# Kernel tuning notes

Hardware: AMD Instinct MI355X
Metric: run time of the kernel (lower is better)

Reference implementation:

```python
import jax, jax.numpy as jnp
import numpy as np

N, QLEN, KLEN = 4, 2048, 2048
QDIM = KVDIM = 512
EMBED, HEADS = 1024, 16
HEAD_DIM = EMBED // HEADS


def setup_inputs() -> dict:
    key = jax.random.key(0)
    ks = jax.random.split(key, 7)
    return {
        "queries": jax.random.normal(ks[0], (N, QLEN, QDIM), dtype=jnp.float32),
        "keys": jax.random.normal(ks[1], (1, KLEN, KVDIM), dtype=jnp.float32),
        "values": jax.random.normal(ks[2], (1, KLEN, KVDIM), dtype=jnp.float32),
        "mask": jax.random.randint(ks[3], (N, 1, 1, KLEN), 0, 2, dtype=jnp.int32),
        "Wq": jax.random.normal(ks[4], (QDIM, EMBED), dtype=jnp.float32) * (QDIM ** -0.5),
        "Wk": jax.random.normal(ks[5], (KVDIM, EMBED), dtype=jnp.float32) * (KVDIM ** -0.5),
        "Wv": jax.random.normal(ks[6], (KVDIM, EMBED), dtype=jnp.float32) * (KVDIM ** -0.5),
    }


def reference(queries, keys, values, mask, Wq, Wk, Wv):
    # Projections (Linear, no bias)
    q = (queries @ Wq).reshape(N, QLEN, HEADS, HEAD_DIM)      # [N, Q, H, D]
    k = (keys @ Wk).reshape(KLEN, HEADS, HEAD_DIM)            # [K, H, D] (batch-1, shared)
    v = (values @ Wv).reshape(KLEN, HEADS, HEAD_DIM)          # [K, H, D]

    # energy: [N, H, Q, K]
    energy = jnp.einsum('nqhd,khd->nhqk', q, k)
    energy = jnp.where(mask == 0, jnp.float32(-1e20), energy)
    attn = jax.nn.softmax(energy / jnp.float32(HEAD_DIM ** 0.5), axis=3)

    out = jnp.einsum('nhqk,khd->nqhd', attn, v)               # [N, Q, H, D]
    return out.reshape(N, QLEN, EMBED)
```

## Files before the change

kernel.cpp:

```cpp
#include <hip/hip_runtime.h>

#define NB 4
#define QLEN 2048
#define KLEN 2048
#define QDIM 512
#define EMBED 1024
#define HEADS 16
#define HD 64

typedef __bf16 bf16x8 __attribute__((ext_vector_type(8)));
typedef float f32x2 __attribute__((ext_vector_type(2)));
typedef float f32x4 __attribute__((ext_vector_type(4)));
typedef float f32x16 __attribute__((ext_vector_type(16)));

#define CLOG 0.18033688011112042f

__device__ __forceinline__ float fexp2(float x) {
#if __has_builtin(__builtin_amdgcn_exp2f)
    return __builtin_amdgcn_exp2f(x);
#else
    float r;
    asm("v_exp_f32 %0, %1\n\ts_nop 1" : "=v"(r) : "v"(x));
    return r;
#endif
}

#if __has_builtin(__builtin_amdgcn_sched_barrier)
#define SCHED_FENCE() __builtin_amdgcn_sched_barrier(0)
#else
#define SCHED_FENCE()
#endif

__device__ __forceinline__ void dma16(const void* g, void* l) {
    __builtin_amdgcn_global_load_lds(
        (const __attribute__((address_space(1))) void*)g,
        (__attribute__((address_space(3))) void*)l, 16, 0, 0);
}

__global__ __launch_bounds__(256) void prep(const float* __restrict__ q,
                                            const float* __restrict__ k,
                                            const float* __restrict__ v,
                                            const float* __restrict__ Wq,
                                            const float* __restrict__ Wk,
                                            const float* __restrict__ Wv,
                                            const int* __restrict__ mask,
                                            __bf16* __restrict__ qd,
                                            __bf16* __restrict__ kd,
                                            __bf16* __restrict__ vd,
                                            __bf16* __restrict__ WtQ,
                                            __bf16* __restrict__ WtK,
                                            __bf16* __restrict__ WtV,
                                            int* __restrict__ pidx,
                                            int* __restrict__ cntg,
                                            __bf16* __restrict__ kbf,
                                            __bf16* __restrict__ vtbf) {
    __shared__ float tile[32][33];
    __shared__ int part[256];
    int b = blockIdx.x, tid = threadIdx.x;
    if (b >= 4612) {
        int t2 = b - 4612, n = t2 >> 4, h = t2 & 15;
        const int* mp = mask + n * KLEN + tid * 8;
        int4 ma = *(const int4*)&mp[0];
        int4 mb = *(const int4*)&mp[4];
        int c = (ma.x != 0) + (ma.y != 0) + (ma.z != 0) + (ma.w != 0)
              + (mb.x != 0) + (mb.y != 0) + (mb.z != 0) + (mb.w != 0);
        part[tid] = c;
        __syncthreads();
        for (int off = 128; off > 0; off >>= 1) {
            if (tid < off) part[tid] += part[tid + off];
            __syncthreads();
        }
        int cnt = part[0];
        int tiles = (cnt + 63) >> 6, pe = tiles << 6, np = pe - cnt;
        __bf16* kb0 = kbf + (((size_t)(n * HEADS + h)) * KLEN + cnt) * HD;
        __bf16* vb0 = vtbf + ((size_t)(n * HEADS + h)) * HD * KLEN;
        for (int i = tid; i < np * HD; i += 256) {
            int r = i >> 6, d = i & 63;
            kb0[r * HD + d] = (__bf16)0.f;
        }
        for (int d = 0; d < HD; d++)
            if (tid < np) vb0[(size_t)d * KLEN + cnt + tid] = (__bf16)0.f;
    } else if (b >= 4608) {
        int n = b - 4608;
        const int* mp = mask + n * KLEN + tid * 8;
        int4 ma = *(const int4*)&mp[0];
        int4 mb = *(const int4*)&mp[4];
        int m[8] = { ma.x, ma.y, ma.z, ma.w, mb.x, mb.y, mb.z, mb.w };
        int c = 0;
#pragma unroll
        for (int j = 0; j < 8; j++) c += (m[j] != 0);
        part[tid] = c;
        __syncthreads();
        for (int off = 1; off < 256; off <<= 1) {
            int vv = (tid >= off) ? part[tid - off] : 0;
            __syncthreads();
            part[tid] += vv;
            __syncthreads();
        }
        int pos = part[tid] - c;
        int* pw = pidx + n * KLEN + tid * 8;
#pragma unroll
        for (int j = 0; j < 8; j++) {
            pw[j] = m[j] ? pos : -1;
            pos += (m[j] != 0);
        }
        if (tid == 0) cntg[n] = part[255];
    } else if (b < 3072) {
        const float* src; __bf16* dst; int cb;
        if (b < 2048)      { src = q; dst = qd; cb = b; }
        else if (b < 2560) { src = k; dst = kd; cb = b - 2048; }
        else               { src = v; dst = vd; cb = b - 2560; }
        int i = (cb * 256 + tid) * 8;
        float4 a0 = *(const float4*)&src[i];
        float4 a1 = *(const float4*)&src[i + 4];
        bf16x8 o;
        o[0] = (__bf16)a0.x; o[1] = (__bf16)a0.y; o[2] = (__bf16)a0.z; o[3] = (__bf16)a0.w;
        o[4] = (__bf16)a1.x; o[5] = (__bf16)a1.y; o[6] = (__bf16)a1.z; o[7] = (__bf16)a1.w;
        *(bf16x8*)&dst[i] = o;
    } else {
        int tb = b - 3072;
        int which = tb >> 9, r = tb & 511;
        const float* src = (which == 0) ? Wq : (which == 1) ? Wk : Wv;
        __bf16* dst = (which == 0) ? WtQ : (which == 1) ? WtK : WtV;
        float scale = (which == 0) ? CLOG : 1.0f;
        int e0 = (r & 31) * 32, c0 = (r >> 5) * 32;
        int tx = tid & 31, ty = tid >> 5;
        for (int i = 0; i < 4; i++)
            tile[ty + 8 * i][tx] = src[(c0 + ty + 8 * i) * EMBED + e0 + tx];
        __syncthreads();
        for (int i = 0; i < 4; i++)
            dst[(e0 + ty + 8 * i) * QDIM + c0 + tx] = (__bf16)(tile[tx][ty + 8 * i] * scale);
    }
}

__device__ __forceinline__ void gemm_compute(const __bf16* As, const __bf16* Bs,
                                             int wr, int wc, int r16, int qq,
                                             f32x4 (&acc)[4][4]) {
    bf16x8 af[4], bq[4];
#pragma unroll
    for (int i = 0; i < 4; i++)
        af[i] = *(const bf16x8*)&As[(wr * 64 + i * 16 + r16) * 32 + qq * 8];
#pragma unroll
    for (int j = 0; j < 4; j++)
        bq[j] = *(const bf16x8*)&Bs[(wc * 64 + j * 16 + r16) * 32 + qq * 8];
#pragma unroll
    for (int i = 0; i < 4; i++)
#pragma unroll
        for (int j = 0; j < 4; j++)
            acc[i][j] = __builtin_amdgcn_mfma_f32_16x16x32_bf16(af[i], bq[j], acc[i][j], 0, 0, 0);
}

__device__ __forceinline__ void gemm128(const __bf16* __restrict__ A,
                                        const __bf16* __restrict__ Bt,
                                        __bf16* As0, __bf16* As1,
                                        __bf16* Bs0, __bf16* Bs1,
                                        int row0, int col0, f32x4 (&acc)[4][4]) {
    int tid = threadIdx.x, wave = tid >> 6, lane = tid & 63;
    int r16 = lane & 15, qq = lane >> 4;
    int wr = wave >> 1, wc = wave & 1;
    const __bf16* agp1 = A + (size_t)(row0 + (tid >> 2)) * QDIM + (tid & 3) * 8;
    const __bf16* agp2 = A + (size_t)(row0 + 64 + (tid >> 2)) * QDIM + (tid & 3) * 8;
    const __bf16* bgp1 = Bt + (size_t)(col0 + (tid >> 2)) * QDIM + (tid & 3) * 8;
    const __bf16* bgp2 = Bt + (size_t)(col0 + 64 + (tid >> 2)) * QDIM + (tid & 3) * 8;
    __bf16 *a0a = &As0[wave * 512], *a0b = &As0[2048 + wave * 512];
    __bf16 *a1a = &As1[wave * 512], *a1b = &As1[2048 + wave * 512];
    __bf16 *b0a = &Bs0[wave * 512], *b0b = &Bs0[2048 + wave * 512];
    __bf16 *b1a = &Bs1[wave * 512], *b1b = &Bs1[2048 + wave * 512];

    dma16(agp1, a0a); dma16(agp2, a0b);
    dma16(bgp1, b0a); dma16(bgp2, b0b);
    agp1 += 32; agp2 += 32; bgp1 += 32; bgp2 += 32;
    __syncthreads();

    for (int t = 0; t < 16; t += 2) {
        dma16(agp1, a1a); dma16(agp2, a1b);
        dma16(bgp1, b1a); dma16(bgp2, b1b);
        agp1 += 32; agp2 += 32; bgp1 += 32; bgp2 += 32;
        SCHED_FENCE();
        gemm_compute(As0, Bs0, wr, wc, r16, qq, acc);
        __syncthreads();
        if (t + 2 < 16) {
            dma16(agp1, a0a); dma16(agp2, a0b);
            dma16(bgp1, b0a); dma16(bgp2, b0b);
            agp1 += 32; agp2 += 32; bgp1 += 32; bgp2 += 32;
        }
        SCHED_FENCE();
        gemm_compute(As1, Bs1, wr, wc, r16, qq, acc);
        __syncthreads();
    }
}

__global__ __launch_bounds__(256) void proj_all(const __bf16* __restrict__ qin,
                                                const __bf16* __restrict__ kin,
                                                const __bf16* __restrict__ vin,
                                                const __bf16* __restrict__ wtq,
                                                const __bf16* __restrict__ wtk,
                                                const __bf16* __restrict__ wtv,
                                                const int* __restrict__ pidx,
                                                __bf16* __restrict__ qout,
                                                __bf16* __restrict__ kout,
                                                __bf16* __restrict__ vtout) {
    __shared__ __align__(16) __bf16 As[2][128 * 32];
    __shared__ __align__(16) __bf16 Bs[2][128 * 32];
    int bid = blockIdx.x;
    const __bf16 *A, *Bt;
    int mode, b;
    if (bid < 512)      { A = qin; Bt = wtq; mode = 0; b = bid; }
    else if (bid < 640) { A = kin; Bt = wtk; mode = 1; b = bid - 512; }
    else                { A = wtv; Bt = vin; mode = 2; b = bid - 640; }
    int row0, col0;
    if (mode == 2) { row0 = (b >> 4) * 128; col0 = (b & 15) * 128; }
    else           { row0 = (b >> 3) * 128; col0 = (b & 7) * 128; }
    f32x4 acc[4][4] = {};
    gemm128(A, Bt, As[0], As[1], Bs[0], Bs[1], row0, col0, acc);
    int lane = threadIdx.x & 63, wave = threadIdx.x >> 6;
    int r16 = lane & 15, qq = lane >> 4;
    int wr = wave >> 1, wc = wave & 1;

    if (mode == 0) {
#pragma unroll
        for (int i = 0; i < 4; i++)
#pragma unroll
            for (int j = 0; j < 4; j++)
#pragma unroll
                for (int rr = 0; rr < 4; rr++) {
                    int grow = row0 + wr * 64 + i * 16 + qq * 4 + rr;
                    int gcol = col0 + wc * 64 + j * 16 + r16;
                    int hh = gcol >> 6, d = gcol & 63;
                    int n = grow >> 11, qr = grow & 2047;
                    qout[((size_t)(n * HEADS + hh) * QLEN + qr) * HD + d] =
                        (__bf16)acc[i][j][rr];
                }
    } else if (mode == 1) {
#pragma unroll
        for (int i = 0; i < 4; i++) {
            int grow0 = row0 + wr * 64 + i * 16 + qq * 4;
            int4 p4[NB];
#pragma unroll
            for (int nn = 0; nn < NB; nn++)
                p4[nn] = *(const int4*)&pidx[nn * KLEN + grow0];
#pragma unroll
            for (int j = 0; j < 4; j++) {
                int gcol = col0 + wc * 64 + j * 16 + r16;
                int hh = gcol >> 6, d = gcol & 63;
#pragma unroll
                for (int rr = 0; rr < 4; rr++) {
                    __bf16 v = (__bf16)acc[i][j][rr];
#pragma unroll
                    for (int nn = 0; nn < NB; nn++) {
                        int p = ((const int*)&p4[nn])[rr];
                        if (p >= 0)
                            kout[((size_t)(nn * HEADS + hh) * KLEN + p) * HD + d] = v;
                    }
                }
            }
        }
    } else {
        int p2[NB][4];
#pragma unroll
        for (int nn = 0; nn < NB; nn++)
#pragma unroll
            for (int j = 0; j < 4; j++)
                p2[nn][j] = pidx[nn * KLEN + col0 + wc * 64 + j * 16 + r16];
#pragma unroll
        for (int i = 0; i < 4; i++)
#pragma unroll
            for (int j = 0; j < 4; j++)
#pragma unroll
                for (int rr = 0; rr < 4; rr++) {
                    int grow = row0 + wr * 64 + i * 16 + qq * 4 + rr;
                    __bf16 v = (__bf16)acc[i][j][rr];
#pragma unroll
                    for (int nn = 0; nn < NB; nn++) {
                        int p = p2[nn][j];
                        if (p >= 0)
                            vtout[((size_t)nn * EMBED + grow) * KLEN + p] = v;
                    }
                }
    }
}

__device__ __forceinline__ void attn_tile(const __bf16* ksb, const __bf16* vsb,
                                          const bf16x8 (&qfrag)[4],
                                          int col, int h,
                                          f32x16& o0, f32x16& o1, f32x2& rsl) {
    bf16x8 pfrag[4];
#pragma unroll
    for (int kt2 = 0; kt2 < 2; kt2++) {
        int R = kt2 * 32 + col;
        f32x16 s = {};
        __builtin_amdgcn_s_setprio(1);
#pragma unroll
        for (int c = 0; c < 4; c++) {
            int cc = (2 * c + h) ^ (R & 7);
            bf16x8 kf = *(const bf16x8*)&ksb[(R * 8 + cc) * 8];
            s = __builtin_amdgcn_mfma_f32_32x32x16_bf16(kf, qfrag[c], s, 0, 0, 0);
        }
        __builtin_amdgcn_s_setprio(0);
#pragma unroll
        for (int G = 0; G < 4; G++) {
            int ci = 2 * kt2 + (G >> 1), e0 = (G & 1) * 4;
#pragma unroll
            for (int rr = 0; rr < 4; rr += 2) {
                float p0 = fexp2(s[4 * G + rr]);
                float p1 = fexp2(s[4 * G + rr + 1]);
                f32x2 pp; pp[0] = p0; pp[1] = p1;
                rsl += pp;
                pfrag[ci][e0 + rr] = (__bf16)p0;
                pfrag[ci][e0 + rr + 1] = (__bf16)p1;
            }
        }
    }
    __builtin_amdgcn_s_setprio(1);
#pragma unroll
    for (int c = 0; c < 4; c++) {
        int cc = (2 * c + h) ^ (col & 7);
        bf16x8 v0 = *(const bf16x8*)&vsb[(col * 8 + cc) * 8];
        bf16x8 v1 = *(const bf16x8*)&vsb[((32 + col) * 8 + cc) * 8];
        o0 = __builtin_amdgcn_mfma_f32_32x32x16_bf16(v0, pfrag[c], o0, 0, 0, 0);
        o1 = __builtin_amdgcn_mfma_f32_32x32x16_bf16(v1, pfrag[c], o1, 0, 0, 0);
    }
    __builtin_amdgcn_s_setprio(0);
}

__global__ __launch_bounds__(512, 4) void attn_kernel(const __bf16* __restrict__ qb,
                                                      const __bf16* __restrict__ kb,
                                                      const __bf16* __restrict__ vtb,
                                                      const int* __restrict__ cntg,
                                                      float* __restrict__ out) {
    __shared__ __align__(16) __bf16 ks[2][4096];
    __shared__ __align__(16) __bf16 vs[2][4096];

    int tid = threadIdx.x, wave = tid >> 6, lane = tid & 63;
    int col = lane & 31, h = lane >> 5;
    int bid = blockIdx.x;
    int qx = bid >> 6, r6 = bid & 63, hh = r6 >> 2, n = r6 & 3;
    int q0 = qx * 256;
    int cnt = cntg[n];
    int tiles = (cnt + 63) >> 6;
    int npad = (tiles << 6) - cnt;
    const __bf16* qg = qb + ((size_t)(n * HEADS + hh) * QLEN + q0 + wave * 32 + col) * HD;
    const __bf16* kg = kb + (size_t)(n * HEADS + hh) * KLEN * HD;
    const __bf16* vg = vtb + (size_t)(n * HEADS + hh) * HD * KLEN;

    bf16x8 qfrag[4];
#pragma unroll
    for (int c = 0; c < 4; c++) qfrag[c] = *(const bf16x8*)&qg[c * 16 + h * 8];

    int R1 = tid >> 3, c1 = (tid & 7) ^ (R1 & 7);
    int g1 = (R1 & 0x33) | ((R1 & 4) << 1) | ((R1 & 8) >> 1);
    const __bf16* kgp1 = kg + g1 * HD + c1 * 8;
    const __bf16* vgp1 = vg + (size_t)R1 * KLEN + c1 * 8;

    dma16(kgp1, &ks[0][wave * 512]); dma16(vgp1, &vs[0][wave * 512]);
    kgp1 += 64 * HD; vgp1 += 64;
    __syncthreads();

    f32x16 o0 = {}, o1 = {};
    f32x2 rsl = {};

    for (int t = 0; t < tiles; t++) {
        int pc = t & 1, pn = pc ^ 1;
        if (t + 1 < tiles) {
            dma16(kgp1, &ks[pn][wave * 512]); dma16(vgp1, &vs[pn][wave * 512]);
            kgp1 += 64 * HD; vgp1 += 64;
        }
        SCHED_FENCE();
        attn_tile(ks[pc], vs[pc], qfrag, col, h, o0, o1, rsl);
        __syncthreads();
    }

    float rs = rsl[0] + rsl[1];
    rs += __shfl_xor(rs, 32);
    rs -= (float)npad;
    float inv = 1.0f / rs;
    float* op = out + ((size_t)n * QLEN + q0 + wave * 32 + col) * EMBED + hh * HD;
#pragma unroll
    for (int G = 0; G < 4; G++) {
        float4 t0, t1;
        t0.x = o0[4 * G + 0] * inv; t0.y = o0[4 * G + 1] * inv;
        t0.z = o0[4 * G + 2] * inv; t0.w = o0[4 * G + 3] * inv;
        t1.x = o1[4 * G + 0] * inv; t1.y = o1[4 * G + 1] * inv;
        t1.z = o1[4 * G + 2] * inv; t1.w = o1[4 * G + 3] * inv;
        *(float4*)&op[8 * G + 4 * h] = t0;
        *(float4*)&op[32 + 8 * G + 4 * h] = t1;
    }
}

extern "C" void kernel_launch(void* const* d_in, const int* in_sizes, int n_in,
                              void* d_out, int out_size, void* d_ws, size_t ws_size,
                              hipStream_t stream) {
    const float* queries = (const float*)d_in[0];
    const float* keys    = (const float*)d_in[1];
    const float* values  = (const float*)d_in[2];
    const int*   mask    = (const int*)d_in[3];
    const float* Wq      = (const float*)d_in[4];
    const float* Wk      = (const float*)d_in[5];
    const float* Wv      = (const float*)d_in[6];
    float* out = (float*)d_out;

    const size_t MiB = 1048576;
    char* ws = (char*)d_ws;
    __bf16* qbf   = (__bf16*)(ws);
    __bf16* kbf   = (__bf16*)(ws + 16 * MiB);
    __bf16* vtbf  = (__bf16*)(ws + 32 * MiB);
    __bf16* wtq   = (__bf16*)(ws + 48 * MiB);
    __bf16* wtk   = (__bf16*)(ws + 49 * MiB);
    __bf16* wtv   = (__bf16*)(ws + 50 * MiB);
    __bf16* qin   = (__bf16*)(ws + 51 * MiB);
    __bf16* kin   = (__bf16*)(ws + 59 * MiB);
    __bf16* vin   = (__bf16*)(ws + 61 * MiB);
    int*    pidx  = (int*)(ws + 63 * MiB);
    int*    cntg  = (int*)(ws + 63 * MiB + 65536);

    prep<<<4676, 256, 0, stream>>>(queries, keys, values, Wq, Wk, Wv, mask,
                                   qin, kin, vin, wtq, wtk, wtv,
                                   pidx, cntg, kbf, vtbf);
    proj_all<<<768, 256, 0, stream>>>(qin, kin, vin, wtq, wtk, wtv, pidx,
                                      qbf, kbf, vtbf);
    attn_kernel<<<512, 512, 0, stream>>>(qbf, kbf, vtbf, cntg, out);
}
```

Baseline: 169.9 us.

## Stage V-projection tile in LDS and write compacted V^T with vectorized stores

The prep kernel now also emits an inverse index (compacted position to key column) and per-128-column prefix starts for each batch mask. The V-projection epilogue first stages its 128x128 output tile in shared memory, then gathers the kept columns and writes contiguous 8-element bf16 vectors into the compacted transposed V buffer, instead of scattered 2-byte stores per batch. Block order is also changed so V and K projection tiles are dispatched before Q tiles. This adds index arrays, an extra LDS round trip and a barrier, plus head/tail handling for unaligned ranges.

```diff
diff --git a/kernel.cpp b/kernel.cpp
--- a/kernel.cpp
+++ b/kernel.cpp
@@ -53,7 +53,9 @@
                                             int* __restrict__ pidx,
                                             int* __restrict__ cntg,
                                             __bf16* __restrict__ kbf,
-                                            __bf16* __restrict__ vtbf) {
+                                            __bf16* __restrict__ vtbf,
+                                            int* __restrict__ cidx,
+                                            int* __restrict__ pst) {
     __shared__ float tile[32][33];
     __shared__ int part[256];
     int b = blockIdx.x, tid = threadIdx.x;
@@ -99,11 +101,15 @@
         }
         int pos = part[tid] - c;
         int* pw = pidx + n * KLEN + tid * 8;
+        int* cw = cidx + n * KLEN;
 #pragma unroll
         for (int j = 0; j < 8; j++) {
             pw[j] = m[j] ? pos : -1;
+            if (m[j]) cw[pos] = tid * 8 + j;
             pos += (m[j] != 0);
         }
+        if ((tid & 15) == 0) pst[n * 17 + (tid >> 4)] = part[tid] - c;
+        if (tid == 255) pst[n * 17 + 16] = part[255];
         if (tid == 0) cntg[n] = part[255];
     } else if (b < 3072) {
         const float* src; __bf16* dst; int cb;
@@ -197,23 +203,25 @@
                                                 const __bf16* __restrict__ wtk,
                                                 const __bf16* __restrict__ wtv,
                                                 const int* __restrict__ pidx,
+                                                const int* __restrict__ cidx,
+                                                const int* __restrict__ pst,
                                                 __bf16* __restrict__ qout,
                                                 __bf16* __restrict__ kout,
                                                 __bf16* __restrict__ vtout) {
-    __shared__ __align__(16) __bf16 As[2][128 * 32];
-    __shared__ __align__(16) __bf16 Bs[2][128 * 32];
+    __shared__ __align__(16) __bf16 smem[16384];
     int bid = blockIdx.x;
     const __bf16 *A, *Bt;
-    int mode, b;
-    if (bid < 512)      { A = qin; Bt = wtq; mode = 0; b = bid; }
-    else if (bid < 640) { A = kin; Bt = wtk; mode = 1; b = bid - 512; }
-    else                { A = wtv; Bt = vin; mode = 2; b = bid - 640; }
-    int row0, col0;
-    if (mode == 2) { row0 = (b >> 4) * 128; col0 = (b & 15) * 128; }
-    else           { row0 = (b >> 3) * 128; col0 = (b & 7) * 128; }
+    int mode, b, row0, col0;
+    if (bid < 128)      { A = wtv; Bt = vin; mode = 2; b = bid;
+                          row0 = (b >> 4) * 128; col0 = (b & 15) * 128; }
+    else if (bid < 256) { A = kin; Bt = wtk; mode = 1; b = bid - 128;
+                          row0 = (b >> 3) * 128; col0 = (b & 7) * 128; }
+    else                { A = qin; Bt = wtq; mode = 0; b = bid - 256;
+                          row0 = (b >> 3) * 128; col0 = (b & 7) * 128; }
     f32x4 acc[4][4] = {};
-    gemm128(A, Bt, As[0], As[1], Bs[0], Bs[1], row0, col0, acc);
-    int lane = threadIdx.x & 63, wave = threadIdx.x >> 6;
+    gemm128(A, Bt, smem, smem + 4096, smem + 8192, smem + 12288, row0, col0, acc);
+    int tid = threadIdx.x;
+    int lane = tid & 63, wave = tid >> 6;
     int r16 = lane & 15, qq = lane >> 4;
     int wr = wave >> 1, wc = wave & 1;
 
@@ -256,27 +264,68 @@
             }
         }
     } else {
-        int p2[NB][4];
-#pragma unroll
-        for (int nn = 0; nn < NB; nn++)
+        __bf16* Ct = smem;
+#pragma unroll
+        for (int i = 0; i < 4; i++)
 #pragma unroll
             for (int j = 0; j < 4; j++)
-                p2[nn][j] = pidx[nn * KLEN + col0 + wc * 64 + j * 16 + r16];
-#pragma unroll
-        for (int i = 0; i < 4; i++)
-#pragma unroll
-            for (int j = 0; j < 4; j++)
 #pragma unroll
                 for (int rr = 0; rr < 4; rr++) {
-                    int grow = row0 + wr * 64 + i * 16 + qq * 4 + rr;
-                    __bf16 v = (__bf16)acc[i][j][rr];
-#pragma unroll
-                    for (int nn = 0; nn < NB; nn++) {
-                        int p = p2[nn][j];
-                        if (p >= 0)
-                            vtout[((size_t)nn * EMBED + grow) * KLEN + p] = v;
+                    int row = wr * 64 + i * 16 + qq * 4 + rr;
+                    int colx = wc * 64 + j * 16 + r16;
+                    Ct[row * 128 + colx] = (__bf16)acc[i][j][rr];
+                }
+        __syncthreads();
+        int ci0 = col0 >> 7;
+        for (int nn = 0; nn < NB; nn++) {
+            int pstart = pst[nn * 17 + ci0];
+            int pend   = pst[nn * 17 + ci0 + 1];
+            int cv = pend - pstart;
+            if (cv <= 0) continue;
+            const int* cix = cidx + nn * KLEN;
+            __bf16* vbase = vtout + (size_t)(nn * EMBED + row0) * KLEN;
+            int p0a = (pstart + 7) & ~7;
+            int p1a = pend & ~7;
+            int headEnd = min(p0a, pend);
+            int nh = headEnd - pstart;
+            if (nh > 0) {
+                int r = tid & 7;
+                if (r < nh) {
+                    int p = pstart + r;
+                    int kk = cix[p] - col0;
+                    for (int e = tid >> 3; e < 128; e += 32)
+                        vbase[(size_t)e * KLEN + p] = Ct[e * 128 + kk];
+                }
+            }
+            if (p1a > p0a) {
+                int nch = (p1a - p0a) >> 3;
+                for (int ch = tid & 31; ch < nch; ch += 32) {
+                    int p = p0a + ch * 8;
+                    int4 ca = *(const int4*)&cix[p];
+                    int4 cb = *(const int4*)&cix[p + 4];
+                    int k0 = ca.x - col0, k1 = ca.y - col0, k2 = ca.z - col0, k3 = ca.w - col0;
+                    int k4 = cb.x - col0, k5 = cb.y - col0, k6 = cb.z - col0, k7 = cb.w - col0;
+                    for (int e = tid >> 5; e < 128; e += 8) {
+                        const __bf16* cr = &Ct[e * 128];
+                        bf16x8 o;
+                        o[0] = cr[k0]; o[1] = cr[k1]; o[2] = cr[k2]; o[3] = cr[k3];
+                        o[4] = cr[k4]; o[5] = cr[k5]; o[6] = cr[k6]; o[7] = cr[k7];
+                        *(bf16x8*)&vbase[(size_t)e * KLEN + p] = o;
                     }
                 }
+            }
+            int t0 = max(p1a, headEnd);
+            int nt = pend - t0;
+            if (nt > 0) {
+                int r = tid & 7;
+                if (r < nt) {
+                    int p = t0 + r;
+                    int kk = cix[p] - col0;
+                    for (int e = tid >> 3; e < 128; e += 32)
+                        vbase[(size_t)e * KLEN + p] = Ct[e * 128 + kk];
+                }
+            }
+        }
     }
 }
 
@@ -412,11 +461,13 @@
     __bf16* vin   = (__bf16*)(ws + 61 * MiB);
     int*    pidx  = (int*)(ws + 63 * MiB);
     int*    cntg  = (int*)(ws + 63 * MiB + 65536);
+    int*    cidx  = (int*)(ws + 63 * MiB + 131072);
+    int*    pst   = (int*)(ws + 63 * MiB + 196608);
 
     prep<<<4676, 256, 0, stream>>>(queries, keys, values, Wq, Wk, Wv, mask,
                                    qin, kin, vin, wtq, wtk, wtv,
-                                   pidx, cntg, kbf, vtbf);
-    proj_all<<<768, 256, 0, stream>>>(qin, kin, vin, wtq, wtk, wtv, pidx,
-                                      qbf, kbf, vtbf);
+                                   pidx, cntg, kbf, vtbf, cidx, pst);
+    proj_all<<<768, 256, 0, stream>>>(qin, kin, vin, wtq, wtk, wtv,
+                                      pidx, cidx, pst, qbf, kbf, vtbf);
     attn_kernel<<<512, 512, 0, stream>>>(qbf, kbf, vtbf, cntg, out);
 }
```

After: 161.0 us. -5.2%, faster.
